# Kernel optimization log

Hardware: AMD Instinct MI355X
Metric: run time of the kernel (lower is better)

Reference implementation:

```python
import jax, jax.numpy as jnp
import numpy as np

NB_CLASSES = 1024
SZ_EMBED = 128
N_SAMPLES = 262144
MRG = 0.1
ALPHA = 32.0


def l2_norm(x):
    # matches torch l2_norm: divide by sqrt(sum(x^2, dim=1) + 1e-12)
    return x / jnp.sqrt(jnp.sum(x * x, axis=1, keepdims=True) + 1e-12)


def setup_inputs() -> dict:
    key = jax.random.key(0)
    k1, k2, k3 = jax.random.split(key, 3)
    X = jax.random.normal(k1, (N_SAMPLES, SZ_EMBED), dtype=jnp.float32)
    proxies = jax.random.normal(k2, (NB_CLASSES, SZ_EMBED), dtype=jnp.float32)
    T = jax.random.randint(k3, (N_SAMPLES,), 0, NB_CLASSES)
    return {"X": X, "proxies": proxies, "T": T}


def reference(X, proxies, T):
    # cosine similarities: [N, C]
    cos = l2_norm(X) @ l2_norm(proxies).T
    # on-device one-hot replaces the numpy binarize roundtrip
    P_one_hot = jax.nn.one_hot(T, NB_CLASSES, dtype=cos.dtype)  # [N, C]
    pos_exp_w = jnp.exp(-ALPHA * (cos - MRG)) * P_one_hot
    neg_exp_w = jnp.exp(ALPHA * (cos + MRG)) * (1.0 - P_one_hot)
    P_sim_sum = pos_exp_w.sum(axis=0)  # [C]
    N_sim_sum = neg_exp_w.sum(axis=0)  # [C]
    num_valid = (P_one_hot.sum(axis=0) != 0).sum().astype(cos.dtype)
    pos_term = jnp.where(
        num_valid > 0,
        jnp.log1p(P_sim_sum).sum() / jnp.maximum(num_valid, 1.0),
        jnp.zeros((), cos.dtype),
    )
    neg_term = jnp.log1p(N_sim_sum).sum() / NB_CLASSES
    loss = pos_term + neg_term
    return jnp.stack([loss, pos_term, neg_term])
```

## Files before the change

### kernel.cpp

```cpp
#include <hip/hip_runtime.h>
#include <math.h>

#define NB_CLASSES 1024
#define SZ_EMBED 128
#define N_SAMPLES 262144
#define MTILE 64
#define CTILE 64
#define NBLOCKS (N_SAMPLES / MTILE)
#define XSTRIDE 136

typedef __bf16 v8bf __attribute__((ext_vector_type(8)));
typedef float v4f __attribute__((ext_vector_type(4)));

#define EXP_A 46.16624130844683f
#define EXP_B 4.616624130844683f

__device__ __forceinline__ unsigned short f2bf(float f) {
    union { float f; unsigned u; } v; v.f = f;
    unsigned u = v.u;
    unsigned rounding = 0x7FFFu + ((u >> 16) & 1u);
    return (unsigned short)((u + rounding) >> 16);
}
__device__ __forceinline__ float bfbits_lo(unsigned u) {
    union { unsigned u; float f; } v; v.u = u << 16; return v.f;
}
__device__ __forceinline__ float bfbits_hi(unsigned u) {
    union { unsigned u; float f; } v; v.u = u & 0xffff0000u; return v.f;
}

__global__ __launch_bounds__(256) void norm_proxies_kernel(
    const float* __restrict__ proxies, unsigned short* __restrict__ pn) {
    int wv = threadIdx.x >> 6;
    int lane = threadIdx.x & 63;
    int row = blockIdx.x * 4 + wv;
    const float* src = proxies + (size_t)row * SZ_EMBED + lane * 2;
    float2 x = *(const float2*)src;
    float ss = x.x * x.x + x.y * x.y;
    #pragma unroll
    for (int off = 32; off; off >>= 1) ss += __shfl_xor(ss, off);
    float inv = rsqrtf(ss + 1e-12f);
    unsigned pk = (unsigned)f2bf(x.x * inv) | ((unsigned)f2bf(x.y * inv) << 16);
    *(unsigned*)(pn + (size_t)row * SZ_EMBED + lane * 2) = pk;
}

__global__ __launch_bounds__(256, 1) void main_kernel(
    const float* __restrict__ X, const int* __restrict__ T,
    const unsigned short* __restrict__ Pn,
    float* __restrict__ partial_neg, float* __restrict__ partial_pos) {
    __shared__ unsigned short xtile[MTILE * XSTRIDE];
    __shared__ float psum[MTILE][4];
    __shared__ float dsum[MTILE][4];
    __shared__ int tT[MTILE];
    __shared__ float neg_lds[NB_CLASSES];
    __shared__ float pos_lds[NB_CLASSES];

    const int t = threadIdx.x;
    const int lane = t & 63;
    const int wv = t >> 6;
    const int quad = lane >> 4;
    const int l15 = lane & 15;
    const int sample_base = blockIdx.x * MTILE;

    *(float4*)(neg_lds + 4 * t) = float4{0.f, 0.f, 0.f, 0.f};
    *(float4*)(pos_lds + 4 * t) = float4{0.f, 0.f, 0.f, 0.f};

    const int row = t >> 2, part = t & 3;
    {
        const float4* src = (const float4*)(X + (size_t)(sample_base + row) * SZ_EMBED + part * 32);
        float4 r[8];
        float ss = 0.f;
        #pragma unroll
        for (int j = 0; j < 8; ++j) {
            r[j] = src[j];
            ss += r[j].x * r[j].x + r[j].y * r[j].y + r[j].z * r[j].z + r[j].w * r[j].w;
        }
        psum[row][part] = ss;
        if (t < MTILE) tT[t] = T[sample_base + t];
        __syncthreads();
        float inv = rsqrtf(psum[row][0] + psum[row][1] + psum[row][2] + psum[row][3] + 1e-12f);
        unsigned short* dst = xtile + row * XSTRIDE + part * 32;
        #pragma unroll
        for (int j = 0; j < 8; ++j) {
            uint2 pk;
            pk.x = (unsigned)f2bf(r[j].x * inv) | ((unsigned)f2bf(r[j].y * inv) << 16);
            pk.y = (unsigned)f2bf(r[j].z * inv) | ((unsigned)f2bf(r[j].w * inv) << 16);
            *(uint2*)(dst + j * 4) = pk;
        }
        int lbl = tT[row];
        const unsigned short* prow = Pn + (size_t)lbl * SZ_EMBED + part * 32;
        float d = 0.f;
        #pragma unroll
        for (int j = 0; j < 4; ++j) {
            uint4 pv = *(const uint4*)(prow + j * 8);
            float4 xa = r[2 * j], xb = r[2 * j + 1];
            d += bfbits_lo(pv.x) * xa.x + bfbits_hi(pv.x) * xa.y;
            d += bfbits_lo(pv.y) * xa.z + bfbits_hi(pv.y) * xa.w;
            d += bfbits_lo(pv.z) * xb.x + bfbits_hi(pv.z) * xb.y;
            d += bfbits_lo(pv.w) * xb.z + bfbits_hi(pv.w) * xb.w;
        }
        dsum[row][part] = d * inv;
    }
    __syncthreads();

    if (part == 0) {
        int lbl = tT[row];
        float dd = dsum[row][0] + dsum[row][1] + dsum[row][2] + dsum[row][3];
        float pos_e = __builtin_amdgcn_exp2f(fmaf(dd, -EXP_A, EXP_B));
        float neg_e = __builtin_amdgcn_exp2f(fmaf(dd,  EXP_A, EXP_B));
        atomicAdd(&pos_lds[lbl], pos_e);
        atomicAdd(&neg_lds[lbl], -neg_e);
    }

    v8bf afrag[4][4];
    #pragma unroll
    for (int ri = 0; ri < 4; ++ri)
        #pragma unroll
        for (int kc = 0; kc < 4; ++kc)
            afrag[ri][kc] = *(const v8bf*)(xtile + (ri * 16 + l15) * XSTRIDE + kc * 32 + quad * 8);

    const unsigned short* bptr = Pn + (size_t)(wv * 16 + l15) * SZ_EMBED + quad * 8;
    v8bf bfrag[2][4];
    #pragma unroll
    for (int kc = 0; kc < 4; ++kc)
        bfrag[0][kc] = *(const v8bf*)(bptr + kc * 32);

    #pragma unroll 2
    for (int ct = 0; ct < NB_CLASSES / CTILE; ++ct) {
        int cur = ct & 1;
        if (ct < NB_CLASSES / CTILE - 1) {
            const unsigned short* nb = bptr + (size_t)(ct + 1) * CTILE * SZ_EMBED;
            #pragma unroll
            for (int kc = 0; kc < 4; ++kc)
                bfrag[cur ^ 1][kc] = *(const v8bf*)(nb + kc * 32);
        }
        v4f zero = {0.f, 0.f, 0.f, 0.f};
        v4f acc[4] = {zero, zero, zero, zero};
        #pragma unroll
        for (int kc = 0; kc < 4; ++kc)
            #pragma unroll
            for (int ri = 0; ri < 4; ++ri)
                acc[ri] = __builtin_amdgcn_mfma_f32_16x16x32_bf16(afrag[ri][kc], bfrag[cur][kc], acc[ri], 0, 0, 0);

        float e[16];
        #pragma unroll
        for (int ri = 0; ri < 4; ++ri)
            #pragma unroll
            for (int r = 0; r < 4; ++r)
                e[ri * 4 + r] = __builtin_amdgcn_exp2f(fmaf(acc[ri][r], EXP_A, EXP_B));
        #pragma unroll
        for (int s = 8; s; s >>= 1)
            #pragma unroll
            for (int j = 0; j < s; ++j)
                e[j] += e[j + s];
        atomicAdd(&neg_lds[ct * CTILE + wv * 16 + l15], e[0]);
    }
    __syncthreads();

    float* nrow = partial_neg + (size_t)blockIdx.x * NB_CLASSES;
    float* prow = partial_pos + (size_t)blockIdx.x * NB_CLASSES;
    *(float4*)(nrow + 4 * t) = *(const float4*)(neg_lds + 4 * t);
    *(float4*)(prow + 4 * t) = *(const float4*)(pos_lds + 4 * t);
}

__global__ __launch_bounds__(256) void row_reduce_kernel(
    float* __restrict__ partial_neg, float* __restrict__ partial_pos,
    int nrows, int rstride) {
    const int t = threadIdx.x;
    const size_t base = (size_t)blockIdx.x * nrows * rstride * NB_CLASSES;
    float4 an = {0.f, 0.f, 0.f, 0.f}, ap = {0.f, 0.f, 0.f, 0.f};
    for (int r = 0; r < nrows; ++r) {
        const float* nrow = partial_neg + base + (size_t)r * rstride * NB_CLASSES;
        const float* prow = partial_pos + base + (size_t)r * rstride * NB_CLASSES;
        float4 vn = *(const float4*)(nrow + 4 * t);
        float4 vp = *(const float4*)(prow + 4 * t);
        an.x += vn.x; an.y += vn.y; an.z += vn.z; an.w += vn.w;
        ap.x += vp.x; ap.y += vp.y; ap.z += vp.z; ap.w += vp.w;
    }
    *(float4*)(partial_neg + base + 4 * t) = an;
    *(float4*)(partial_pos + base + 4 * t) = ap;
}

__global__ __launch_bounds__(256) void finalize_kernel(
    const float* __restrict__ partial_neg, const float* __restrict__ partial_pos,
    float* __restrict__ out) {
    int t = threadIdx.x;
    float4 ns = {0.f, 0.f, 0.f, 0.f}, ps = {0.f, 0.f, 0.f, 0.f};
    #pragma unroll
    for (int r = 0; r < 16; ++r) {
        float4 vn = *(const float4*)(partial_neg + (size_t)r * 256 * NB_CLASSES + 4 * t);
        float4 vp = *(const float4*)(partial_pos + (size_t)r * 256 * NB_CLASSES + 4 * t);
        ns.x += vn.x; ns.y += vn.y; ns.z += vn.z; ns.w += vn.w;
        ps.x += vp.x; ps.y += vp.y; ps.z += vp.z; ps.w += vp.w;
    }
    float lp_pos = log1pf(ps.x) + log1pf(ps.y) + log1pf(ps.z) + log1pf(ps.w);
    float lp_neg = log1pf(ns.x) + log1pf(ns.y) + log1pf(ns.z) + log1pf(ns.w);
    float valid = (ps.x != 0.f) + (ps.y != 0.f) + (ps.z != 0.f) + (ps.w != 0.f);
    #pragma unroll
    for (int off = 32; off; off >>= 1) {
        lp_pos += __shfl_xor(lp_pos, off);
        lp_neg += __shfl_xor(lp_neg, off);
        valid  += __shfl_xor(valid, off);
    }
    __shared__ float s[3][4];
    int wv = t >> 6, lane = t & 63;
    if (lane == 0) { s[0][wv] = lp_pos; s[1][wv] = lp_neg; s[2][wv] = valid; }
    __syncthreads();
    if (t == 0) {
        float P = s[0][0] + s[0][1] + s[0][2] + s[0][3];
        float Ng = s[1][0] + s[1][1] + s[1][2] + s[1][3];
        float V = s[2][0] + s[2][1] + s[2][2] + s[2][3];
        float pos_term = (V > 0.f) ? (P / fmaxf(V, 1.f)) : 0.f;
        float neg_term = Ng / (float)NB_CLASSES;
        out[0] = pos_term + neg_term;
        out[1] = pos_term;
        out[2] = neg_term;
    }
}

extern "C" void kernel_launch(void* const* d_in, const int* in_sizes, int n_in,
                              void* d_out, int out_size, void* d_ws, size_t ws_size,
                              hipStream_t stream) {
    const float* X = (const float*)d_in[0];
    const float* proxies = (const float*)d_in[1];
    const int* T = (const int*)d_in[2];
    float* out = (float*)d_out;

    char* ws = (char*)d_ws;
    unsigned short* Pn = (unsigned short*)ws;
    float* partial_neg = (float*)(ws + (size_t)NB_CLASSES * SZ_EMBED * sizeof(unsigned short));
    float* partial_pos = partial_neg + (size_t)NBLOCKS * NB_CLASSES;

    norm_proxies_kernel<<<NB_CLASSES / 4, 256, 0, stream>>>(proxies, Pn);
    main_kernel<<<NBLOCKS, 256, 0, stream>>>(X, T, Pn, partial_neg, partial_pos);
    row_reduce_kernel<<<256, 256, 0, stream>>>(partial_neg, partial_pos, 16, 1);
    row_reduce_kernel<<<16, 256, 0, stream>>>(partial_neg, partial_pos, 16, 16);
    finalize_kernel<<<1, 256, 0, stream>>>(partial_neg, partial_pos, out);
}
```

Before: 313.8 us.

## Alias LDS accumulators over X tile and use single-pass row reduction

```diff
diff --git a/kernel.cpp b/kernel.cpp
--- a/kernel.cpp
+++ b/kernel.cpp
@@ -14,6 +14,8 @@
 
 #define EXP_A 46.16624130844683f
 #define EXP_B 4.616624130844683f
+
+#define SMEM_BYTES 19712
 
 __device__ __forceinline__ unsigned short f2bf(float f) {
     union { float f; unsigned u; } v; v.f = f;
@@ -47,12 +49,13 @@
     const float* __restrict__ X, const int* __restrict__ T,
     const unsigned short* __restrict__ Pn,
     float* __restrict__ partial_neg, float* __restrict__ partial_pos) {
-    __shared__ unsigned short xtile[MTILE * XSTRIDE];
-    __shared__ float psum[MTILE][4];
-    __shared__ float dsum[MTILE][4];
-    __shared__ int tT[MTILE];
-    __shared__ float neg_lds[NB_CLASSES];
-    __shared__ float pos_lds[NB_CLASSES];
+    __shared__ __align__(16) char smem[SMEM_BYTES];
+    unsigned short* xtile = (unsigned short*)smem;
+    float (*psum)[4] = (float(*)[4])(smem + 17408);
+    float (*dsum)[4] = (float(*)[4])(smem + 18432);
+    int* tT = (int*)(smem + 19456);
+    float* neg_lds = (float*)smem;
+    float* pos_lds = (float*)(smem + 4096);
 
     const int t = threadIdx.x;
     const int lane = t & 63;
@@ -60,9 +63,6 @@
     const int quad = lane >> 4;
     const int l15 = lane & 15;
     const int sample_base = blockIdx.x * MTILE;
-
-    *(float4*)(neg_lds + 4 * t) = float4{0.f, 0.f, 0.f, 0.f};
-    *(float4*)(pos_lds + 4 * t) = float4{0.f, 0.f, 0.f, 0.f};
 
     const int row = t >> 2, part = t & 3;
     {
@@ -102,21 +102,31 @@
     }
     __syncthreads();
 
-    if (part == 0) {
-        int lbl = tT[row];
-        float dd = dsum[row][0] + dsum[row][1] + dsum[row][2] + dsum[row][3];
-        float pos_e = __builtin_amdgcn_exp2f(fmaf(dd, -EXP_A, EXP_B));
-        float neg_e = __builtin_amdgcn_exp2f(fmaf(dd,  EXP_A, EXP_B));
-        atomicAdd(&pos_lds[lbl], pos_e);
-        atomicAdd(&neg_lds[lbl], -neg_e);
-    }
-
     v8bf afrag[4][4];
     #pragma unroll
     for (int ri = 0; ri < 4; ++ri)
         #pragma unroll
         for (int kc = 0; kc < 4; ++kc)
             afrag[ri][kc] = *(const v8bf*)(xtile + (ri * 16 + l15) * XSTRIDE + kc * 32 + quad * 8);
+
+    float diag_pos = 0.f, diag_neg = 0.f;
+    int diag_lbl = 0;
+    if (part == 0) {
+        diag_lbl = tT[row];
+        float dd = dsum[row][0] + dsum[row][1] + dsum[row][2] + dsum[row][3];
+        diag_pos = __builtin_amdgcn_exp2f(fmaf(dd, -EXP_A, EXP_B));
+        diag_neg = __builtin_amdgcn_exp2f(fmaf(dd,  EXP_A, EXP_B));
+    }
+    __syncthreads();
+
+    *(float4*)(neg_lds + 4 * t) = float4{0.f, 0.f, 0.f, 0.f};
+    *(float4*)(pos_lds + 4 * t) = float4{0.f, 0.f, 0.f, 0.f};
+    __syncthreads();
+
+    if (part == 0) {
+        atomicAdd(&pos_lds[diag_lbl], diag_pos);
+        atomicAdd(&neg_lds[diag_lbl], -diag_neg);
+    }
 
     const unsigned short* bptr = Pn + (size_t)(wv * 16 + l15) * SZ_EMBED + quad * 8;
     v8bf bfrag[2][4];
@@ -163,14 +173,13 @@
 }
 
 __global__ __launch_bounds__(256) void row_reduce_kernel(
-    float* __restrict__ partial_neg, float* __restrict__ partial_pos,
-    int nrows, int rstride) {
+    float* __restrict__ partial_neg, float* __restrict__ partial_pos) {
     const int t = threadIdx.x;
-    const size_t base = (size_t)blockIdx.x * nrows * rstride * NB_CLASSES;
+    const size_t base = (size_t)blockIdx.x * 64 * NB_CLASSES;
     float4 an = {0.f, 0.f, 0.f, 0.f}, ap = {0.f, 0.f, 0.f, 0.f};
-    for (int r = 0; r < nrows; ++r) {
-        const float* nrow = partial_neg + base + (size_t)r * rstride * NB_CLASSES;
-        const float* prow = partial_pos + base + (size_t)r * rstride * NB_CLASSES;
+    for (int r = 0; r < 64; ++r) {
+        const float* nrow = partial_neg + base + (size_t)r * NB_CLASSES;
+        const float* prow = partial_pos + base + (size_t)r * NB_CLASSES;
         float4 vn = *(const float4*)(nrow + 4 * t);
         float4 vp = *(const float4*)(prow + 4 * t);
         an.x += vn.x; an.y += vn.y; an.z += vn.z; an.w += vn.w;
@@ -185,10 +194,10 @@
     float* __restrict__ out) {
     int t = threadIdx.x;
     float4 ns = {0.f, 0.f, 0.f, 0.f}, ps = {0.f, 0.f, 0.f, 0.f};
-    #pragma unroll
-    for (int r = 0; r < 16; ++r) {
-        float4 vn = *(const float4*)(partial_neg + (size_t)r * 256 * NB_CLASSES + 4 * t);
-        float4 vp = *(const float4*)(partial_pos + (size_t)r * 256 * NB_CLASSES + 4 * t);
+    #pragma unroll 8
+    for (int r = 0; r < 64; ++r) {
+        float4 vn = *(const float4*)(partial_neg + (size_t)r * 64 * NB_CLASSES + 4 * t);
+        float4 vp = *(const float4*)(partial_pos + (size_t)r * 64 * NB_CLASSES + 4 * t);
         ns.x += vn.x; ns.y += vn.y; ns.z += vn.z; ns.w += vn.w;
         ps.x += vp.x; ps.y += vp.y; ps.z += vp.z; ps.w += vp.w;
     }
@@ -232,7 +241,6 @@
 
     norm_proxies_kernel<<<NB_CLASSES / 4, 256, 0, stream>>>(proxies, Pn);
     main_kernel<<<NBLOCKS, 256, 0, stream>>>(X, T, Pn, partial_neg, partial_pos);
-    row_reduce_kernel<<<256, 256, 0, stream>>>(partial_neg, partial_pos, 16, 1);
-    row_reduce_kernel<<<16, 256, 0, stream>>>(partial_neg, partial_pos, 16, 16);
+    row_reduce_kernel<<<64, 256, 0, stream>>>(partial_neg, partial_pos);
     finalize_kernel<<<1, 256, 0, stream>>>(partial_neg, partial_pos, out);
 }
```

Result: no change. 316.4 us (+0.8%).
